# Optimization experiments

Hardware: AMD Instinct MI355X
Metric: run time of the kernel (lower is better)

The kernel has to match this reference:

```python
import jax, jax.numpy as jnp
import numpy as np

B, T, D, H, HS = 4, 1024, 1024, 16, 64
DW, DA, DG, DV = 64, 64, 128, 32
DM = H * HS  # == D here
EPS = 1e-5
DECAY_C = -0.606531  # -exp(-0.5)


def setup_inputs() -> dict:
    key = jax.random.key(0)
    ks = jax.random.split(key, 24)
    n = lambda k, s: jax.random.normal(k, s, dtype=jnp.float32)
    w = lambda k, s: n(k, s) * (1.0 / np.sqrt(s[0]))
    return dict(
        current=n(ks[0], (B, T, D)),
        prev=n(ks[1], (B, T, D)),
        v_first=n(ks[2], (B, T, DM)),
        rwkvag=jax.random.uniform(ks[3], (6, D), dtype=jnp.float32),
        rw_W=w(ks[4], (D, D)),
        w1=w(ks[5], (D, DW)), w2=w(ks[6], (DW, DM)), w2_b=n(ks[7], (DM,)) * 0.1,
        kw_W=w(ks[8], (D, DM)), vw_W=w(ks[9], (D, DM)),
        a1=w(ks[10], (D, DA)), a2=w(ks[11], (DA, DM)), a2_b=n(ks[12], (DM,)) * 0.1,
        v1=w(ks[13], (D, DV)), v2=w(ks[14], (DV, DM)), v2_b=n(ks[15], (DM,)) * 0.1,
        g1=w(ks[16], (D, DG)), g2=w(ks[17], (DG, DM)), g2_b=n(ks[18], (DM,)) * 0.1,
        k_k=jnp.ones((DM,)), k_a=jax.random.uniform(ks[19], (DM,), dtype=jnp.float32),
        r_k=jnp.ones((DM,)),
        gn_scale=jnp.ones((DM,)), gn_bias=jnp.zeros((DM,)),
        out_W=w(ks[20], (DM, D)),
    )


def _add_heads(x):
    return x.reshape(x.shape[:-1] + (H, HS))


def reference(current, prev, v_first, rwkvag, rw_W, w1, w2, w2_b, kw_W, vw_W,
              a1, a2, a2_b, v1, v2, v2_b, g1, g2, g2_b,
              k_k, k_a, r_k, gn_scale, gn_bias, out_W):
    diff = prev - current
    # per-channel token-shift mixing for the 6 branches: (B,T,6,D)
    x6 = current[..., None, :] + rwkvag * diff[..., None, :]
    xr, xw, xk, xv, xa, xg = (x6[..., i, :] for i in range(6))

    r = xr @ rw_W
    wl = jnp.tanh(xw @ w1) @ w2 + w2_b          # w-LoRA (tanh, bias_post)
    k = xk @ kw_W
    v = xv @ vw_W
    a = jax.nn.sigmoid((xa @ a1) @ a2 + a2_b)   # a-LoRA (bias_post) + sigmoid
    g = jax.nn.sigmoid(xg @ g1) @ g2 + g2_b     # g-LoRA (sigmoid act)

    kk = _add_heads(k * k_k)
    kk = kk / jnp.linalg.norm(kk, axis=-1, keepdims=True)
    k = k * (1.0 + (a - 1.0) * k_a)
    v = v + (v_first - v) * jax.nn.sigmoid((xv @ v1) @ v2 + v2_b)
    wdec = jnp.exp(DECAY_C * jax.nn.sigmoid(wl))  # decay in (exp(-0.6065), 1)

    rk_sum = _add_heads(r * k * r_k).sum(-1, keepdims=True)  # (B,T,H,1)
    rh, wh, kh, vh = _add_heads(r), _add_heads(wdec), _add_heads(k), _add_heads(v)
    at = -kk
    bt = kk * _add_heads(a)

    def step(state, xs):
        rt, wt, ktt, vt, att, btt = xs  # each (B,H,HS)
        sa = jnp.einsum('bhvk,bhk->bhv', state, att)
        state = (state * wt[:, :, None, :]
                 + sa[..., None] * btt[:, :, None, :]
                 + vt[..., None] * ktt[:, :, None, :])
        y = jnp.einsum('bhvk,bhk->bhv', state, rt)
        return state, y

    xs = tuple(jnp.moveaxis(x, 1, 0) for x in (rh, wh, kh, vh, at, bt))
    state0 = jnp.zeros((B, H, HS, HS), dtype=current.dtype)
    state, ys = jax.lax.scan(step, state0, xs)
    out = jnp.moveaxis(ys, 0, 1)  # (B,T,H,HS)

    # GroupNorm with n_head groups (normalize within each head)
    mu = out.mean(-1, keepdims=True)
    var = out.var(-1, keepdims=True)
    outn = (out - mu) * jax.lax.rsqrt(var + EPS)
    outn = outn.reshape(B, T, DM) * gn_scale + gn_bias

    outn = outn + (rk_sum * vh).reshape(B, T, DM)
    y = (outn * g) @ out_W
    return y, state, v_first
```

## Files before the change

### kernel.cpp

```cpp
#include <hip/hip_runtime.h>
#include <math.h>

#define NT 4096
#define DD 1024
#define NH 16
#define HSZ 64
#define GN_EPS 1e-5f
#define DECAY_C -0.606531f

typedef __attribute__((ext_vector_type(8))) short short8;
typedef __attribute__((ext_vector_type(4))) float float4v;

#define GLB(p) ((const __attribute__((address_space(1))) void*)(p))
#define LDS(p) ((__attribute__((address_space(3))) void*)(p))

__device__ __forceinline__ float sigm(float x) { return 1.f / (1.f + __expf(-x)); }

__device__ __forceinline__ unsigned short f2bf(float f) {
    unsigned int u = __float_as_uint(f);
    u = (u + 0x7fffu + ((u >> 16) & 1u)) >> 16;
    return (unsigned short)u;
}
__device__ __forceinline__ float bf2f(unsigned short h) {
    return __uint_as_float(((unsigned int)h) << 16);
}

__device__ __forceinline__ float row_sum16(float x) {
    int t;
    t = __builtin_amdgcn_update_dpp(0, __float_as_int(x), 0x128, 0xF, 0xF, true);
    x += __int_as_float(t);
    t = __builtin_amdgcn_update_dpp(0, __float_as_int(x), 0x124, 0xF, 0xF, true);
    x += __int_as_float(t);
    t = __builtin_amdgcn_update_dpp(0, __float_as_int(x), 0x122, 0xF, 0xF, true);
    x += __int_as_float(t);
    t = __builtin_amdgcn_update_dpp(0, __float_as_int(x), 0x121, 0xF, 0xF, true);
    x += __int_as_float(t);
    return x;
}

__global__ __launch_bounds__(256)
void mix6(const float* __restrict__ cur, const float* __restrict__ prev,
          const float* __restrict__ lam,
          ushort* __restrict__ xrh, ushort* __restrict__ xrl,
          ushort* __restrict__ xwh, ushort* __restrict__ xwl,
          ushort* __restrict__ xkh, ushort* __restrict__ xkl,
          ushort* __restrict__ xvh, ushort* __restrict__ xvl,
          ushort* __restrict__ xah, ushort* __restrict__ xal,
          ushort* __restrict__ xgh, ushort* __restrict__ xgl)
{
    const int tok = blockIdx.x;
    const int d0 = threadIdx.x * 4;
    const size_t base = (size_t)tok * DD + d0;
    float4 c = *(const float4*)(cur + base);
    float4 p = *(const float4*)(prev + base);
    float dx = p.x - c.x, dy = p.y - c.y, dz = p.z - c.z, dw = p.w - c.w;
    ushort* hs[6] = {xrh, xwh, xkh, xvh, xah, xgh};
    ushort* ls[6] = {xrl, xwl, xkl, xvl, xal, xgl};
#pragma unroll
    for (int j = 0; j < 6; j++) {
        float4 l = *(const float4*)(lam + j * DD + d0);
        float m0 = c.x + l.x * dx;
        float m1 = c.y + l.y * dy;
        float m2 = c.z + l.z * dz;
        float m3 = c.w + l.w * dw;
        ushort4 h;
        h.x = f2bf(m0); h.y = f2bf(m1); h.z = f2bf(m2); h.w = f2bf(m3);
        *(ushort4*)(hs[j] + base) = h;
        ushort4 lo;
        lo.x = f2bf(m0 - bf2f(h.x));
        lo.y = f2bf(m1 - bf2f(h.y));
        lo.z = f2bf(m2 - bf2f(h.z));
        lo.w = f2bf(m3 - bf2f(h.w));
        *(ushort4*)(ls[j] + base) = lo;
    }
}

__global__ __launch_bounds__(256)
void transpose_pad(const float* __restrict__ W, ushort* __restrict__ Wh,
                   ushort* __restrict__ Wl, int K, int N)
{
    __shared__ float tile[32][33];
    const int bx = blockIdx.x * 32;
    const int by = blockIdx.y * 32;
    const int tx = threadIdx.x, ty = threadIdx.y;
#pragma unroll
    for (int i = 0; i < 32; i += 8) {
        float v = 0.f;
        if (bx + tx < N) v = W[(size_t)(by + ty + i) * N + bx + tx];
        tile[ty + i][tx] = v;
    }
    __syncthreads();
#pragma unroll
    for (int i = 0; i < 32; i += 8) {
        float v = tile[tx][ty + i];
        ushort h = f2bf(v);
        size_t o = (size_t)(bx + ty + i) * K + by + tx;
        Wh[o] = h;
        if (Wl) Wl[o] = f2bf(v - bf2f(h));
    }
}

#define SWZ(r) (((r) >> 1) & 3)

__global__ __launch_bounds__(256)
void gemm_mega1(const ushort* __restrict__ xrh, const ushort* __restrict__ xrl,
                const ushort* __restrict__ xwh, const ushort* __restrict__ xwl,
                const ushort* __restrict__ xkh, const ushort* __restrict__ xkl,
                const ushort* __restrict__ xvh, const ushort* __restrict__ xvl,
                const ushort* __restrict__ xah, const ushort* __restrict__ xal,
                const ushort* __restrict__ xgh, const ushort* __restrict__ xgl,
                const ushort* __restrict__ Bth, const ushort* __restrict__ Btl,
                float* __restrict__ r_buf, float* __restrict__ k_buf,
                float* __restrict__ v_buf,
                ushort* __restrict__ hwh, ushort* __restrict__ hwl,
                ushort* __restrict__ hah, ushort* __restrict__ hal,
                ushort* __restrict__ hvh, ushort* __restrict__ hvl,
                ushort* __restrict__ hgh, ushort* __restrict__ hgl)
{
    __shared__ ushort AsH[128 * 32];
    __shared__ ushort BsH[128 * 32];
    __shared__ ushort AsL[128 * 32];
    __shared__ ushort BsL[128 * 32];
    const int cb = blockIdx.y;
    const ushort* Ah; const ushort* Al;
    if (cb < 8)       { Ah = xrh; Al = xrl; }
    else if (cb < 16) { Ah = xkh; Al = xkl; }
    else if (cb < 24) { Ah = xvh; Al = xvl; }
    else if (cb == 24){ Ah = xwh; Al = xwl; }
    else if (cb == 25){ Ah = xah; Al = xal; }
    else if (cb == 26){ Ah = xvh; Al = xvl; }
    else              { Ah = xgh; Al = xgl; }

    const int tid = threadIdx.x;
    const int rowBase = blockIdx.x * 128;
    const int colBase = cb * 128;
    const int lane = tid & 63;
    const int wave = tid >> 6;
    const int wm = wave >> 1, wn = wave & 1;
    const int m15 = lane & 15, quad = lane >> 4;

    float4v zero4 = {0.f, 0.f, 0.f, 0.f};
    float4v acc[4][4];
#pragma unroll
    for (int i = 0; i < 4; i++)
#pragma unroll
        for (int j = 0; j < 4; j++) acc[i][j] = zero4;

    for (int k0 = 0; k0 < 1024; k0 += 32) {
#pragma unroll
        for (int i = 0; i < 2; i++) {
            int idx = i * 256 + tid;
            int r = idx >> 2, seg = idx & 3;
            int sg = seg ^ SWZ(r);
            size_t aoff = (size_t)(rowBase + r) * 1024 + k0 + sg * 8;
            size_t boff = (size_t)(colBase + r) * 1024 + k0 + sg * 8;
            int dst = (i * 256 + (tid & ~63)) * 8;
            __builtin_amdgcn_global_load_lds(GLB(Ah + aoff), LDS(AsH + dst), 16, 0, 0);
            __builtin_amdgcn_global_load_lds(GLB(Bth + boff), LDS(BsH + dst), 16, 0, 0);
            __builtin_amdgcn_global_load_lds(GLB(Al + aoff), LDS(AsL + dst), 16, 0, 0);
            __builtin_amdgcn_global_load_lds(GLB(Btl + boff), LDS(BsL + dst), 16, 0, 0);
        }
        __syncthreads();
        short8 ah[4], bh[4], al[4], bl[4];
#pragma unroll
        for (int mi = 0; mi < 4; mi++) {
            int ra = wm * 64 + mi * 16 + m15;
            int cs = (quad ^ SWZ(ra)) * 8;
            ah[mi] = *(const short8*)(AsH + ra * 32 + cs);
            al[mi] = *(const short8*)(AsL + ra * 32 + cs);
        }
#pragma unroll
        for (int ni = 0; ni < 4; ni++) {
            int rb = wn * 64 + ni * 16 + m15;
            int cs = (quad ^ SWZ(rb)) * 8;
            bh[ni] = *(const short8*)(BsH + rb * 32 + cs);
            bl[ni] = *(const short8*)(BsL + rb * 32 + cs);
        }
#pragma unroll
        for (int mi = 0; mi < 4; mi++)
#pragma unroll
            for (int ni = 0; ni < 4; ni++) {
                acc[mi][ni] = __builtin_amdgcn_mfma_f32_16x16x32_bf16(al[mi], bh[ni], acc[mi][ni], 0, 0, 0);
                acc[mi][ni] = __builtin_amdgcn_mfma_f32_16x16x32_bf16(ah[mi], bl[ni], acc[mi][ni], 0, 0, 0);
                acc[mi][ni] = __builtin_amdgcn_mfma_f32_16x16x32_bf16(ah[mi], bh[ni], acc[mi][ni], 0, 0, 0);
            }
        __syncthreads();
    }

#pragma unroll
    for (int mi = 0; mi < 4; mi++) {
#pragma unroll
        for (int ni = 0; ni < 4; ni++) {
            int c = wn * 64 + ni * 16 + m15;
#pragma unroll
            for (int rr = 0; rr < 4; rr++) {
                int row = rowBase + wm * 64 + mi * 16 + quad * 4 + rr;
                float v = acc[mi][ni][rr];
                if (cb < 24) {
                    float* dst = (cb < 8) ? r_buf : (cb < 16) ? k_buf : v_buf;
                    int n = (cb & 7) * 128 + c;
                    dst[(size_t)row * 1024 + n] = v;
                } else if (cb == 24) {
                    if (c < 64) {
                        float t = tanhf(v);
                        ushort h = f2bf(t);
                        hwh[(size_t)row * 64 + c] = h;
                        hwl[(size_t)row * 64 + c] = f2bf(t - bf2f(h));
                    }
                } else if (cb == 25) {
                    if (c < 64) {
                        ushort h = f2bf(v);
                        hah[(size_t)row * 64 + c] = h;
                        hal[(size_t)row * 64 + c] = f2bf(v - bf2f(h));
                    }
                } else if (cb == 26) {
                    if (c < 32) {
                        ushort h = f2bf(v);
                        hvh[(size_t)row * 32 + c] = h;
                        hvl[(size_t)row * 32 + c] = f2bf(v - bf2f(h));
                    }
                } else {
                    float t = sigm(v);
                    ushort h = f2bf(t);
                    hgh[(size_t)row * 128 + c] = h;
                    hgl[(size_t)row * 128 + c] = f2bf(t - bf2f(h));
                }
            }
        }
    }
}

__global__ __launch_bounds__(256)
void gemm_mega2(const ushort* __restrict__ hwh, const ushort* __restrict__ hwl,
                const ushort* __restrict__ hah, const ushort* __restrict__ hal,
                const ushort* __restrict__ hvh, const ushort* __restrict__ hvl,
                const ushort* __restrict__ hgh, const ushort* __restrict__ hgl,
                const ushort* __restrict__ w2Th, const ushort* __restrict__ w2Tl,
                const ushort* __restrict__ a2Th, const ushort* __restrict__ a2Tl,
                const ushort* __restrict__ v2Th, const ushort* __restrict__ v2Tl,
                const ushort* __restrict__ g2Th, const ushort* __restrict__ g2Tl,
                const float* __restrict__ w2_b, const float* __restrict__ a2_b,
                const float* __restrict__ v2_b, const float* __restrict__ g2_b,
                float* __restrict__ w_buf, float* __restrict__ a_buf,
                float* __restrict__ vg_buf, float* __restrict__ g_buf)
{
    __shared__ ushort AsH[128 * 32];
    __shared__ ushort BsH[128 * 32];
    __shared__ ushort AsL[128 * 32];
    __shared__ ushort BsL[128 * 32];
    const int cb = blockIdx.y;
    const int seg = cb >> 3;
    const int K = (seg == 2) ? 32 : (seg == 3) ? 128 : 64;
    const ushort *Ah, *Al, *Bh, *Bl;
    const float* bias;
    float* outp;
    if (seg == 0) { Ah = hwh; Al = hwl; Bh = w2Th; Bl = w2Tl; bias = w2_b; outp = w_buf; }
    else if (seg == 1) { Ah = hah; Al = hal; Bh = a2Th; Bl = a2Tl; bias = a2_b; outp = a_buf; }
    else if (seg == 2) { Ah = hvh; Al = hvl; Bh = v2Th; Bl = v2Tl; bias = v2_b; outp = vg_buf; }
    else { Ah = hgh; Al = hgl; Bh = g2Th; Bl = g2Tl; bias = g2_b; outp = g_buf; }

    const int tid = threadIdx.x;
    const int rowBase = blockIdx.x * 128;
    const int colBase = (cb & 7) * 128;
    const int lane = tid & 63;
    const int wave = tid >> 6;
    const int wm = wave >> 1, wn = wave & 1;
    const int m15 = lane & 15, quad = lane >> 4;

    float4v zero4 = {0.f, 0.f, 0.f, 0.f};
    float4v acc[4][4];
#pragma unroll
    for (int i = 0; i < 4; i++)
#pragma unroll
        for (int j = 0; j < 4; j++) acc[i][j] = zero4;

    for (int k0 = 0; k0 < K; k0 += 32) {
#pragma unroll
        for (int i = 0; i < 2; i++) {
            int idx = i * 256 + tid;
            int r = idx >> 2, s8 = idx & 3;
            int sg = s8 ^ SWZ(r);
            size_t aoff = (size_t)(rowBase + r) * K + k0 + sg * 8;
            size_t boff = (size_t)(colBase + r) * K + k0 + sg * 8;
            int dst = (i * 256 + (tid & ~63)) * 8;
            __builtin_amdgcn_global_load_lds(GLB(Ah + aoff), LDS(AsH + dst), 16, 0, 0);
            __builtin_amdgcn_global_load_lds(GLB(Bh + boff), LDS(BsH + dst), 16, 0, 0);
            __builtin_amdgcn_global_load_lds(GLB(Al + aoff), LDS(AsL + dst), 16, 0, 0);
            __builtin_amdgcn_global_load_lds(GLB(Bl + boff), LDS(BsL + dst), 16, 0, 0);
        }
        __syncthreads();
        short8 ah[4], bh[4], al[4], bl[4];
#pragma unroll
        for (int mi = 0; mi < 4; mi++) {
            int ra = wm * 64 + mi * 16 + m15;
            int cs = (quad ^ SWZ(ra)) * 8;
            ah[mi] = *(const short8*)(AsH + ra * 32 + cs);
            al[mi] = *(const short8*)(AsL + ra * 32 + cs);
        }
#pragma unroll
        for (int ni = 0; ni < 4; ni++) {
            int rb = wn * 64 + ni * 16 + m15;
            int cs = (quad ^ SWZ(rb)) * 8;
            bh[ni] = *(const short8*)(BsH + rb * 32 + cs);
            bl[ni] = *(const short8*)(BsL + rb * 32 + cs);
        }
#pragma unroll
        for (int mi = 0; mi < 4; mi++)
#pragma unroll
            for (int ni = 0; ni < 4; ni++) {
                acc[mi][ni] = __builtin_amdgcn_mfma_f32_16x16x32_bf16(al[mi], bh[ni], acc[mi][ni], 0, 0, 0);
                acc[mi][ni] = __builtin_amdgcn_mfma_f32_16x16x32_bf16(ah[mi], bl[ni], acc[mi][ni], 0, 0, 0);
                acc[mi][ni] = __builtin_amdgcn_mfma_f32_16x16x32_bf16(ah[mi], bh[ni], acc[mi][ni], 0, 0, 0);
            }
        __syncthreads();
    }

#pragma unroll
    for (int mi = 0; mi < 4; mi++) {
#pragma unroll
        for (int ni = 0; ni < 4; ni++) {
            int col = colBase + wn * 64 + ni * 16 + m15;
            float bv = bias[col];
#pragma unroll
            for (int rr = 0; rr < 4; rr++) {
                int row = rowBase + wm * 64 + mi * 16 + quad * 4 + rr;
                float v = acc[mi][ni][rr] + bv;
                if (seg == 1 || seg == 2) v = sigm(v);
                outp[(size_t)row * 1024 + col] = v;
            }
        }
    }
}

__global__ __launch_bounds__(256)
void gemm_bf16s(const ushort* __restrict__ Ah, const ushort* __restrict__ Bh,
                float* __restrict__ outF, int N, int K)
{
    __shared__ ushort AsH[128 * 32];
    __shared__ ushort BsH[128 * 32];
    const int tid = threadIdx.x;
    const int rowBase = blockIdx.x * 128;
    const int colBase = blockIdx.y * 128;
    const int lane = tid & 63;
    const int wave = tid >> 6;
    const int wm = wave >> 1, wn = wave & 1;
    const int m15 = lane & 15, quad = lane >> 4;

    float4v zero4 = {0.f, 0.f, 0.f, 0.f};
    float4v acc[4][4];
#pragma unroll
    for (int i = 0; i < 4; i++)
#pragma unroll
        for (int j = 0; j < 4; j++) acc[i][j] = zero4;

    for (int k0 = 0; k0 < K; k0 += 32) {
#pragma unroll
        for (int i = 0; i < 2; i++) {
            int idx = i * 256 + tid;
            int r = idx >> 2, seg = idx & 3;
            int sg = seg ^ SWZ(r);
            size_t aoff = (size_t)(rowBase + r) * K + k0 + sg * 8;
            size_t boff = (size_t)(colBase + r) * K + k0 + sg * 8;
            int dst = (i * 256 + (tid & ~63)) * 8;
            __builtin_amdgcn_global_load_lds(GLB(Ah + aoff), LDS(AsH + dst), 16, 0, 0);
            __builtin_amdgcn_global_load_lds(GLB(Bh + boff), LDS(BsH + dst), 16, 0, 0);
        }
        __syncthreads();
        short8 ah[4], bh[4];
#pragma unroll
        for (int mi = 0; mi < 4; mi++) {
            int ra = wm * 64 + mi * 16 + m15;
            ah[mi] = *(const short8*)(AsH + ra * 32 + (quad ^ SWZ(ra)) * 8);
        }
#pragma unroll
        for (int ni = 0; ni < 4; ni++) {
            int rb = wn * 64 + ni * 16 + m15;
            bh[ni] = *(const short8*)(BsH + rb * 32 + (quad ^ SWZ(rb)) * 8);
        }
#pragma unroll
        for (int mi = 0; mi < 4; mi++)
#pragma unroll
            for (int ni = 0; ni < 4; ni++)
                acc[mi][ni] = __builtin_amdgcn_mfma_f32_16x16x32_bf16(ah[mi], bh[ni], acc[mi][ni], 0, 0, 0);
        __syncthreads();
    }

#pragma unroll
    for (int mi = 0; mi < 4; mi++) {
#pragma unroll
        for (int ni = 0; ni < 4; ni++) {
            int col = colBase + wn * 64 + ni * 16 + m15;
#pragma unroll
            for (int rr = 0; rr < 4; rr++) {
                int row = rowBase + wm * 64 + mi * 16 + quad * 4 + rr;
                outF[(size_t)row * N + col] = acc[mi][ni][rr];
            }
        }
    }
}

__global__ __launch_bounds__(256)
void elemwise1(const float* __restrict__ r_buf, float* __restrict__ wl_buf,
               float* __restrict__ k_buf, float* __restrict__ v_buf,
               float* __restrict__ kkn_buf, const float* __restrict__ a_buf,
               const float* __restrict__ vg_buf, const float* __restrict__ vfirst,
               const float* __restrict__ kkw, const float* __restrict__ kaw,
               const float* __restrict__ rkw, float* __restrict__ rk_sum)
{
    const int tok = blockIdx.x;
    const int tid = threadIdx.x;
    const int d0 = tid * 4;
    const size_t base = (size_t)tok * DD + d0;

    float4 k0 = *(const float4*)(k_buf + base);
    float4 a4 = *(const float4*)(a_buf + base);
    float4 wl = *(const float4*)(wl_buf + base);
    float4 v0 = *(const float4*)(v_buf + base);
    float4 vg = *(const float4*)(vg_buf + base);
    float4 vf = *(const float4*)(vfirst + base);
    float4 r4 = *(const float4*)(r_buf + base);
    float4 kkc = *(const float4*)(kkw + d0);
    float4 kac = *(const float4*)(kaw + d0);
    float4 rkc = *(const float4*)(rkw + d0);

    float kk0 = k0.x * kkc.x, kk1 = k0.y * kkc.y, kk2 = k0.z * kkc.z, kk3 = k0.w * kkc.w;
    float ss = kk0 * kk0 + kk1 * kk1 + kk2 * kk2 + kk3 * kk3;
    ss += __shfl_xor(ss, 1); ss += __shfl_xor(ss, 2);
    ss += __shfl_xor(ss, 4); ss += __shfl_xor(ss, 8);
    float rn = rsqrtf(ss);
    float4 kkn = { kk0 * rn, kk1 * rn, kk2 * rn, kk3 * rn };
    *(float4*)(kkn_buf + base) = kkn;

    float4 kf;
    kf.x = k0.x * (1.f + (a4.x - 1.f) * kac.x);
    kf.y = k0.y * (1.f + (a4.y - 1.f) * kac.y);
    kf.z = k0.z * (1.f + (a4.z - 1.f) * kac.z);
    kf.w = k0.w * (1.f + (a4.w - 1.f) * kac.w);
    *(float4*)(k_buf + base) = kf;

    float rk = r4.x * kf.x * rkc.x + r4.y * kf.y * rkc.y + r4.z * kf.z * rkc.z + r4.w * kf.w * rkc.w;
    rk += __shfl_xor(rk, 1); rk += __shfl_xor(rk, 2);
    rk += __shfl_xor(rk, 4); rk += __shfl_xor(rk, 8);
    if ((tid & 15) == 0) rk_sum[(size_t)tok * NH + (tid >> 4)] = rk;

    float4 vfin;
    vfin.x = v0.x + (vf.x - v0.x) * vg.x;
    vfin.y = v0.y + (vf.y - v0.y) * vg.y;
    vfin.z = v0.z + (vf.z - v0.z) * vg.z;
    vfin.w = v0.w + (vf.w - v0.w) * vg.w;
    *(float4*)(v_buf + base) = vfin;

    float4 wd;
    wd.x = __expf(DECAY_C * sigm(wl.x));
    wd.y = __expf(DECAY_C * sigm(wl.y));
    wd.z = __expf(DECAY_C * sigm(wl.z));
    wd.w = __expf(DECAY_C * sigm(wl.w));
    *(float4*)(wl_buf + base) = wd;
}

__global__ __launch_bounds__(256)
void scan_kernel(const float* __restrict__ r_buf, const float* __restrict__ w_buf,
                 const float* __restrict__ k_buf, const float* __restrict__ kkn_buf,
                 const float* __restrict__ a_buf, const float* __restrict__ v_buf,
                 float* __restrict__ out_scan, float* __restrict__ state_out)
{
    __shared__ float vecJ[2][5][16][64];
    __shared__ float vbuf2[2][16][16];
    __shared__ float ypart[2][16][16][16];
    const int bh = blockIdx.x;
    const int rg = blockIdx.y;
    const int b = bh >> 4, h = bh & 15;
    const int tid = threadIdx.x;
    const int row = tid >> 4, l16 = tid & 15;
    const int lofs = l16 * 4;
    const int rowbase = rg * 16;
    const size_t tok0 = ((size_t)b * 1024) * DD + h * HSZ;
    float s0 = 0.f, s1 = 0.f, s2 = 0.f, s3 = 0.f;

#define STAGE(cc, bb) do {                                                        \
    const int tt_ = tid >> 4;                                                     \
    const int dd4_ = (tid & 15) * 4;                                              \
    size_t gofs_ = tok0 + (size_t)((cc) * 16 + tt_) * DD + dd4_;                  \
    float* db_ = &vecJ[bb][0][0][0] + ((tid >> 6) << 8);                          \
    __builtin_amdgcn_global_load_lds(GLB(r_buf + gofs_),   LDS(db_),        16, 0, 0); \
    __builtin_amdgcn_global_load_lds(GLB(w_buf + gofs_),   LDS(db_ + 1024), 16, 0, 0); \
    __builtin_amdgcn_global_load_lds(GLB(k_buf + gofs_),   LDS(db_ + 2048), 16, 0, 0); \
    __builtin_amdgcn_global_load_lds(GLB(kkn_buf + gofs_), LDS(db_ + 3072), 16, 0, 0); \
    __builtin_amdgcn_global_load_lds(GLB(a_buf + gofs_),   LDS(db_ + 4096), 16, 0, 0); \
    if (tid < 64) {                                                               \
        size_t vofs_ = tok0 + (size_t)((cc) * 16 + (tid >> 2)) * DD + rowbase + (tid & 3) * 4; \
        __builtin_amdgcn_global_load_lds(GLB(v_buf + vofs_), LDS(&vbuf2[bb][0][0]), 16, 0, 0); \
    }                                                                             \
} while (0)

#define LD_TOK(P, tt) do {                                                        \
    P##r = *(const float4*)(vb + (tt) * 64 + lofs);                               \
    P##w = *(const float4*)(vb + 1024 + (tt) * 64 + lofs);                        \
    P##k = *(const float4*)(vb + 2048 + (tt) * 64 + lofs);                        \
    P##q = *(const float4*)(vb + 3072 + (tt) * 64 + lofs);                        \
    P##a = *(const float4*)(vb + 4096 + (tt) * 64 + lofs);                        \
    P##v = vbp[(tt) * 16 + row];                                                  \
} while (0)

#define STEP(P, tt) do {                                                          \
    float sa_ = P##q.x * s0;                                                      \
    sa_ = fmaf(P##q.y, s1, sa_);                                                  \
    sa_ = fmaf(P##q.z, s2, sa_);                                                  \
    sa_ = fmaf(P##q.w, s3, sa_);                                                  \
    sa_ = row_sum16(sa_);                                                         \
    float n0_ = P##q.x * P##a.x, n1_ = P##q.y * P##a.y;                           \
    float n2_ = P##q.z * P##a.z, n3_ = P##q.w * P##a.w;                           \
    float b0_ = fmaf(s0, P##w.x, P##v * P##k.x);                                  \
    float b1_ = fmaf(s1, P##w.y, P##v * P##k.y);                                  \
    float b2_ = fmaf(s2, P##w.z, P##v * P##k.z);                                  \
    float b3_ = fmaf(s3, P##w.w, P##v * P##k.w);                                  \
    s0 = fmaf(sa_, -n0_, b0_);                                                    \
    s1 = fmaf(sa_, -n1_, b1_);                                                    \
    s2 = fmaf(sa_, -n2_, b2_);                                                    \
    s3 = fmaf(sa_, -n3_, b3_);                                                    \
    float yp_ = P##r.x * s0;                                                      \
    yp_ = fmaf(P##r.y, s1, yp_);                                                  \
    yp_ = fmaf(P##r.z, s2, yp_);                                                  \
    yp_ = fmaf(P##r.w, s3, yp_);                                                  \
    ypart[buf][tt][row][l16] = yp_;                                               \
} while (0)

    STAGE(0, 0);
    __syncthreads();

    for (int c = 0; c < 64; c++) {
        const int buf = c & 1;
        if (c < 63) STAGE(c + 1, buf ^ 1);
        const float* vb  = &vecJ[buf][0][0][0];
        const float* vbp = &vbuf2[buf][0][0];
        float4 Ar, Aw, Ak, Aq, Aa; float Av;
        float4 Br, Bw, Bk, Bq, Ba; float Bv;
        LD_TOK(A, 0);
#pragma unroll
        for (int tp = 0; tp < 8; tp++) {
            LD_TOK(B, 2 * tp + 1);
            STEP(A, 2 * tp);
            if (tp < 7) LD_TOK(A, 2 * tp + 2);
            STEP(B, 2 * tp + 1);
        }
        __syncthreads();
        {
            const int t_ = tid >> 4, r_ = tid & 15;
            const float* yp = &ypart[buf][t_][r_][0];
            float4 y0 = *(const float4*)(yp);
            float4 y1 = *(const float4*)(yp + 4);
            float4 y2 = *(const float4*)(yp + 8);
            float4 y3 = *(const float4*)(yp + 12);
            float ys = ((y0.x + y0.y) + (y0.z + y0.w)) + ((y1.x + y1.y) + (y1.z + y1.w))
                     + ((y2.x + y2.y) + (y2.z + y2.w)) + ((y3.x + y3.y) + (y3.z + y3.w));
            out_scan[tok0 + (size_t)(c * 16 + t_) * DD + rowbase + r_] = ys;
        }
    }

#undef STAGE
#undef LD_TOK
#undef STEP

    float* so = state_out + ((size_t)(b * NH + h) * HSZ + rowbase + row) * HSZ + l16 * 4;
    float4 sv = {s0, s1, s2, s3};
    *(float4*)so = sv;
}

__global__ __launch_bounds__(256)
void elemwise2(const float* __restrict__ out_scan, const float* __restrict__ rk_sum,
               const float* __restrict__ v_buf, const float* __restrict__ g_buf,
               const float* __restrict__ gscale, const float* __restrict__ gbias,
               ushort* __restrict__ z_buf)
{
    const int tok = blockIdx.x;
    const int tid = threadIdx.x;
    const int d0 = tid * 4;
    const size_t base = (size_t)tok * DD + d0;

    float4 o = *(const float4*)(out_scan + base);
    float sm = o.x + o.y + o.z + o.w;
    float ss = o.x * o.x + o.y * o.y + o.z * o.z + o.w * o.w;
    sm += __shfl_xor(sm, 1); sm += __shfl_xor(sm, 2);
    sm += __shfl_xor(sm, 4); sm += __shfl_xor(sm, 8);
    ss += __shfl_xor(ss, 1); ss += __shfl_xor(ss, 2);
    ss += __shfl_xor(ss, 4); ss += __shfl_xor(ss, 8);
    float mu = sm * (1.f / 64.f);
    float var = ss * (1.f / 64.f) - mu * mu;
    float rs = rsqrtf(var + GN_EPS);
    float rk = rk_sum[(size_t)tok * NH + (tid >> 4)];

    float4 v4 = *(const float4*)(v_buf + base);
    float4 g4 = *(const float4*)(g_buf + base);
    float4 gs = *(const float4*)(gscale + d0);
    float4 gb = *(const float4*)(gbias + d0);
    ushort4 z;
    z.x = f2bf(((o.x - mu) * rs * gs.x + gb.x + rk * v4.x) * g4.x);
    z.y = f2bf(((o.y - mu) * rs * gs.y + gb.y + rk * v4.y) * g4.y);
    z.z = f2bf(((o.z - mu) * rs * gs.z + gb.z + rk * v4.z) * g4.z);
    z.w = f2bf(((o.w - mu) * rs * gs.w + gb.w + rk * v4.w) * g4.w);
    *(ushort4*)(z_buf + base) = z;
}

extern "C" void kernel_launch(void* const* d_in, const int* in_sizes, int n_in,
                              void* d_out, int out_size, void* d_ws, size_t ws_size,
                              hipStream_t stream) {
    const float* cur    = (const float*)d_in[0];
    const float* prev   = (const float*)d_in[1];
    const float* vfirst = (const float*)d_in[2];
    const float* rwkvag = (const float*)d_in[3];
    const float* rw_W   = (const float*)d_in[4];
    const float* w1     = (const float*)d_in[5];
    const float* w2     = (const float*)d_in[6];
    const float* w2_b   = (const float*)d_in[7];
    const float* kw_W   = (const float*)d_in[8];
    const float* vw_W   = (const float*)d_in[9];
    const float* a1     = (const float*)d_in[10];
    const float* a2     = (const float*)d_in[11];
    const float* a2_b   = (const float*)d_in[12];
    const float* v1     = (const float*)d_in[13];
    const float* v2     = (const float*)d_in[14];
    const float* v2_b   = (const float*)d_in[15];
    const float* g1     = (const float*)d_in[16];
    const float* g2     = (const float*)d_in[17];
    const float* g2_b   = (const float*)d_in[18];
    const float* k_k    = (const float*)d_in[19];
    const float* k_a    = (const float*)d_in[20];
    const float* r_k    = (const float*)d_in[21];
    const float* gn_s   = (const float*)d_in[22];
    const float* gn_b   = (const float*)d_in[23];
    const float* out_W  = (const float*)d_in[24];

    float* out = (float*)d_out;
    float* y_out = out;
    float* state_out = out + (size_t)NT * DD;
    float* vf_out = state_out + (size_t)4 * NH * HSZ * HSZ;

    float* p = (float*)d_ws;
    const size_t big = (size_t)NT * DD;
    const size_t half = big / 2;
    float* r_buf = p;   p += big;
    float* k_buf = p;   p += big;
    float* v_buf = p;   p += big;
    float* xreg = p;
    ushort* xrh = (ushort*)(xreg);            ushort* xrl = (ushort*)(xreg + half);
    ushort* xwh = (ushort*)(xreg + 2*half);   ushort* xwl = (ushort*)(xreg + 3*half);
    ushort* xkh = (ushort*)(xreg + 4*half);   ushort* xkl = (ushort*)(xreg + 5*half);
    ushort* xvh = (ushort*)(xreg + 6*half);   ushort* xvl = (ushort*)(xreg + 7*half);
    ushort* xah = (ushort*)(xreg + 8*half);   ushort* xal = (ushort*)(xreg + 9*half);
    ushort* xgh = (ushort*)(xreg + 10*half);  ushort* xgl = (ushort*)(xreg + 11*half);
    p += 12 * half;
    float* w_buf   = xreg + 0 * half;
    float* a_buf   = xreg + 2 * half;
    float* vg_buf  = xreg + 4 * half;
    float* os_buf  = vg_buf;
    float* g_buf   = xreg + 6 * half;
    float* kkn_buf = xreg + 8 * half;
    float* btreg = p;
    ushort* Bth = (ushort*)btreg;
    ushort* Btl = (ushort*)(btreg + 1835008);
    p += 2 * 1835008;
    ushort* z_bf  = (ushort*)btreg;
    ushort* outTh = (ushort*)(btreg + 2097152);
    ushort* w2Th = (ushort*)p; p += 32768; ushort* w2Tl = (ushort*)p; p += 32768;
    ushort* a2Th = (ushort*)p; p += 32768; ushort* a2Tl = (ushort*)p; p += 32768;
    ushort* v2Th = (ushort*)p; p += 16384; ushort* v2Tl = (ushort*)p; p += 16384;
    ushort* g2Th = (ushort*)p; p += 65536; ushort* g2Tl = (ushort*)p; p += 65536;
    ushort* hwh = (ushort*)p; p += 131072; ushort* hwl = (ushort*)p; p += 131072;
    ushort* hah = (ushort*)p; p += 131072; ushort* hal = (ushort*)p; p += 131072;
    ushort* hvh = (ushort*)p; p += 65536;  ushort* hvl = (ushort*)p; p += 65536;
    ushort* hgh = (ushort*)p; p += 262144; ushort* hgl = (ushort*)p; p += 262144;
    float* rks_buf = p;        p += 65536;

    dim3 blk(256);
    dim3 t32x8(32, 8);

    transpose_pad<<<dim3(32, 32), t32x8, 0, stream>>>(rw_W, Bth + (size_t)0 * 1024,    Btl + (size_t)0 * 1024,    1024, 1024);
    transpose_pad<<<dim3(32, 32), t32x8, 0, stream>>>(kw_W, Bth + (size_t)1024 * 1024, Btl + (size_t)1024 * 1024, 1024, 1024);
    transpose_pad<<<dim3(32, 32), t32x8, 0, stream>>>(vw_W, Bth + (size_t)2048 * 1024, Btl + (size_t)2048 * 1024, 1024, 1024);
    transpose_pad<<<dim3(4, 32), t32x8, 0, stream>>>(w1, Bth + (size_t)3072 * 1024, Btl + (size_t)3072 * 1024, 1024, 64);
    transpose_pad<<<dim3(4, 32), t32x8, 0, stream>>>(a1, Bth + (size_t)3200 * 1024, Btl + (size_t)3200 * 1024, 1024, 64);
    transpose_pad<<<dim3(4, 32), t32x8, 0, stream>>>(v1, Bth + (size_t)3328 * 1024, Btl + (size_t)3328 * 1024, 1024, 32);
    transpose_pad<<<dim3(4, 32), t32x8, 0, stream>>>(g1, Bth + (size_t)3456 * 1024, Btl + (size_t)3456 * 1024, 1024, 128);
    transpose_pad<<<dim3(32, 2), t32x8, 0, stream>>>(w2, w2Th, w2Tl, 64, 1024);
    transpose_pad<<<dim3(32, 2), t32x8, 0, stream>>>(a2, a2Th, a2Tl, 64, 1024);
    transpose_pad<<<dim3(32, 1), t32x8, 0, stream>>>(v2, v2Th, v2Tl, 32, 1024);
    transpose_pad<<<dim3(32, 4), t32x8, 0, stream>>>(g2, g2Th, g2Tl, 128, 1024);

    mix6<<<NT, blk, 0, stream>>>(cur, prev, rwkvag,
                                 xrh, xrl, xwh, xwl, xkh, xkl,
                                 xvh, xvl, xah, xal, xgh, xgl);

    gemm_mega1<<<dim3(32, 28), blk, 0, stream>>>(
        xrh, xrl, xwh, xwl, xkh, xkl, xvh, xvl, xah, xal, xgh, xgl,
        Bth, Btl, r_buf, k_buf, v_buf,
        hwh, hwl, hah, hal, hvh, hvl, hgh, hgl);

    transpose_pad<<<dim3(32, 32), t32x8, 0, stream>>>(out_W, outTh, nullptr, 1024, 1024);

    gemm_mega2<<<dim3(32, 32), blk, 0, stream>>>(
        hwh, hwl, hah, hal, hvh, hvl, hgh, hgl,
        w2Th, w2Tl, a2Th, a2Tl, v2Th, v2Tl, g2Th, g2Tl,
        w2_b, a2_b, v2_b, g2_b,
        w_buf, a_buf, vg_buf, g_buf);

    elemwise1<<<NT, blk, 0, stream>>>(r_buf, w_buf, k_buf, v_buf, kkn_buf, a_buf,
                                      vg_buf, vfirst, k_k, k_a, r_k, rks_buf);

    scan_kernel<<<dim3(64, 4), blk, 0, stream>>>(r_buf, w_buf, k_buf, kkn_buf, a_buf, v_buf,
                                                 os_buf, state_out);

    elemwise2<<<NT, blk, 0, stream>>>(os_buf, rks_buf, v_buf, g_buf, gn_s, gn_b, z_bf);

    gemm_bf16s<<<dim3(32, 8), blk, 0, stream>>>(z_bf, outTh, y_out, 1024, 1024);

    hipMemcpyAsync(vf_out, vfirst, (size_t)NT * DD * sizeof(float),
                   hipMemcpyDeviceToDevice, stream);
}
```

Measured before the change: 536.7 us.

## Enlarge gemm_mega1 tiles to 256x256 with double-buffered LDS prefetch

The fused first-stage GEMM moves from 128x128 tiles with 256 threads to 256x256 tiles with 512 threads. Each wave now computes a 128x64 sub-tile, and the LDS staging is double-buffered so the next K-slice loads while MFMAs run on the current one. The goal is more operand reuse per byte loaded, fewer blocks, and global-load latency hidden behind compute. In exchange, the small LoRA projections are padded to 256 columns, which adds wasted MFMA work. Each thread holds 128 accumulator floats under a 512-thread, 2-block launch bound, so register spilling or low occupancy is a risk, and LDS use rises to 128 KB per block.

```diff
diff --git a/kernel.cpp b/kernel.cpp
--- a/kernel.cpp
+++ b/kernel.cpp
@@ -102,7 +102,7 @@
 
 #define SWZ(r) (((r) >> 1) & 3)
 
-__global__ __launch_bounds__(256)
+__global__ __launch_bounds__(512, 2)
 void gemm_mega1(const ushort* __restrict__ xrh, const ushort* __restrict__ xrl,
                 const ushort* __restrict__ xwh, const ushort* __restrict__ xwl,
                 const ushort* __restrict__ xkh, const ushort* __restrict__ xkl,
@@ -117,113 +117,127 @@
                 ushort* __restrict__ hvh, ushort* __restrict__ hvl,
                 ushort* __restrict__ hgh, ushort* __restrict__ hgl)
 {
-    __shared__ ushort AsH[128 * 32];
-    __shared__ ushort BsH[128 * 32];
-    __shared__ ushort AsL[128 * 32];
-    __shared__ ushort BsL[128 * 32];
-    const int cb = blockIdx.y;
+    __shared__ ushort As[2][2][256 * 32];
+    __shared__ ushort Bs[2][2][256 * 32];
+    const int ct = blockIdx.y;
     const ushort* Ah; const ushort* Al;
-    if (cb < 8)       { Ah = xrh; Al = xrl; }
-    else if (cb < 16) { Ah = xkh; Al = xkl; }
-    else if (cb < 24) { Ah = xvh; Al = xvl; }
-    else if (cb == 24){ Ah = xwh; Al = xwl; }
-    else if (cb == 25){ Ah = xah; Al = xal; }
-    else if (cb == 26){ Ah = xvh; Al = xvl; }
+    if (ct < 4)       { Ah = xrh; Al = xrl; }
+    else if (ct < 8)  { Ah = xkh; Al = xkl; }
+    else if (ct < 12) { Ah = xvh; Al = xvl; }
+    else if (ct == 12){ Ah = xwh; Al = xwl; }
+    else if (ct == 13){ Ah = xah; Al = xal; }
+    else if (ct == 14){ Ah = xvh; Al = xvl; }
     else              { Ah = xgh; Al = xgl; }
 
     const int tid = threadIdx.x;
-    const int rowBase = blockIdx.x * 128;
-    const int colBase = cb * 128;
+    const int rowBase = blockIdx.x * 256;
+    const int colBase = ct * 256;
     const int lane = tid & 63;
     const int wave = tid >> 6;
-    const int wm = wave >> 1, wn = wave & 1;
+    const int wm = wave >> 2, wn = wave & 3;
     const int m15 = lane & 15, quad = lane >> 4;
 
     float4v zero4 = {0.f, 0.f, 0.f, 0.f};
-    float4v acc[4][4];
-#pragma unroll
-    for (int i = 0; i < 4; i++)
+    float4v acc[8][4];
+#pragma unroll
+    for (int i = 0; i < 8; i++)
 #pragma unroll
         for (int j = 0; j < 4; j++) acc[i][j] = zero4;
 
-    for (int k0 = 0; k0 < 1024; k0 += 32) {
-#pragma unroll
-        for (int i = 0; i < 2; i++) {
-            int idx = i * 256 + tid;
-            int r = idx >> 2, seg = idx & 3;
-            int sg = seg ^ SWZ(r);
-            size_t aoff = (size_t)(rowBase + r) * 1024 + k0 + sg * 8;
-            size_t boff = (size_t)(colBase + r) * 1024 + k0 + sg * 8;
-            int dst = (i * 256 + (tid & ~63)) * 8;
-            __builtin_amdgcn_global_load_lds(GLB(Ah + aoff), LDS(AsH + dst), 16, 0, 0);
-            __builtin_amdgcn_global_load_lds(GLB(Bth + boff), LDS(BsH + dst), 16, 0, 0);
-            __builtin_amdgcn_global_load_lds(GLB(Al + aoff), LDS(AsL + dst), 16, 0, 0);
-            __builtin_amdgcn_global_load_lds(GLB(Btl + boff), LDS(BsL + dst), 16, 0, 0);
-        }
-        __syncthreads();
-        short8 ah[4], bh[4], al[4], bl[4];
-#pragma unroll
-        for (int mi = 0; mi < 4; mi++) {
-            int ra = wm * 64 + mi * 16 + m15;
-            int cs = (quad ^ SWZ(ra)) * 8;
-            ah[mi] = *(const short8*)(AsH + ra * 32 + cs);
-            al[mi] = *(const short8*)(AsL + ra * 32 + cs);
-        }
+#define STAGE1(kk, bb) do {                                                       \
+    const int k0_ = (kk) * 32;                                                    \
+    _Pragma("unroll")                                                             \
+    for (int i_ = 0; i_ < 2; i_++) {                                              \
+        int idx_ = i_ * 512 + tid;                                                \
+        int r_ = idx_ >> 2, seg_ = idx_ & 3;                                      \
+        int sg_ = seg_ ^ SWZ(r_);       \
+        size_t aoff_ = (size_t)(rowBase + r_) * 1024 + k0_ + sg_ * 8;             \
+        size_t boff_ = (size_t)(colBase + r_) * 1024 + k0_ + sg_ * 8;             \
+        int dst_ = (i_ * 512 + (tid & ~63)) * 8;                                  \
+        __builtin_amdgcn_global_load_lds(GLB(Ah + aoff_),  LDS(&As[bb][0][0] + dst_), 16, 0, 0); \
+        __builtin_amdgcn_global_load_lds(GLB(Al + aoff_),  LDS(&As[bb][1][0] + dst_), 16, 0, 0); \
+        __builtin_amdgcn_global_load_lds(GLB(Bth + boff_), LDS(&Bs[bb][0][0] + dst_), 16, 0, 0); \
+        __builtin_amdgcn_global_load_lds(GLB(Btl + boff_), LDS(&Bs[bb][1][0] + dst_), 16, 0, 0); \
+    }                                                                             \
+} while (0)
+
+    STAGE1(0, 0);
+    __syncthreads();
+
+    for (int kt = 0; kt < 32; kt++) {
+        const int buf = kt & 1;
+        if (kt < 31) STAGE1(kt + 1, buf ^ 1);
+
+        short8 bh[4], bl[4];
 #pragma unroll
         for (int ni = 0; ni < 4; ni++) {
             int rb = wn * 64 + ni * 16 + m15;
             int cs = (quad ^ SWZ(rb)) * 8;
-            bh[ni] = *(const short8*)(BsH + rb * 32 + cs);
-            bl[ni] = *(const short8*)(BsL + rb * 32 + cs);
-        }
-#pragma unroll
-        for (int mi = 0; mi < 4; mi++)
-#pragma unroll
-            for (int ni = 0; ni < 4; ni++) {
-                acc[mi][ni] = __builtin_amdgcn_mfma_f32_16x16x32_bf16(al[mi], bh[ni], acc[mi][ni], 0, 0, 0);
-                acc[mi][ni] = __builtin_amdgcn_mfma_f32_16x16x32_bf16(ah[mi], bl[ni], acc[mi][ni], 0, 0, 0);
-                acc[mi][ni] = __builtin_amdgcn_mfma_f32_16x16x32_bf16(ah[mi], bh[ni], acc[mi][ni], 0, 0, 0);
+            bh[ni] = *(const short8*)(&Bs[buf][0][0] + rb * 32 + cs);
+            bl[ni] = *(const short8*)(&Bs[buf][1][0] + rb * 32 + cs);
+        }
+#pragma unroll
+        for (int h2 = 0; h2 < 2; h2++) {
+            short8 ah[4], al[4];
+#pragma unroll
+            for (int mi = 0; mi < 4; mi++) {
+                int ra = wm * 128 + (h2 * 4 + mi) * 16 + m15;
+                int cs = (quad ^ SWZ(ra)) * 8;
+                ah[mi] = *(const short8*)(&As[buf][0][0] + ra * 32 + cs);
+                al[mi] = *(const short8*)(&As[buf][1][0] + ra * 32 + cs);
             }
+#pragma unroll
+            for (int mi = 0; mi < 4; mi++)
+#pragma unroll
+                for (int ni = 0; ni < 4; ni++) {
+                    acc[h2*4+mi][ni] = __builtin_amdgcn_mfma_f32_16x16x32_bf16(al[mi], bh[ni], acc[h2*4+mi][ni], 0, 0, 0);
+                    acc[h2*4+mi][ni] = __builtin_amdgcn_mfma_f32_16x16x32_bf16(ah[mi], bl[ni], acc[h2*4+mi][ni], 0, 0, 0);
+                    acc[h2*4+mi][ni] = __builtin_amdgcn_mfma_f32_16x16x32_bf16(ah[mi], bh[ni], acc[h2*4+mi][ni], 0, 0, 0);
+                }
+        }
         __syncthreads();
     }
-
-#pragma unroll
-    for (int mi = 0; mi < 4; mi++) {
+#undef STAGE1
+
+#pragma unroll
+    for (int mi = 0; mi < 8; mi++) {
 #pragma unroll
         for (int ni = 0; ni < 4; ni++) {
             int c = wn * 64 + ni * 16 + m15;
 #pragma unroll
             for (int rr = 0; rr < 4; rr++) {
-                int row = rowBase + wm * 64 + mi * 16 + quad * 4 + rr;
+                int row = rowBase + wm * 128 + mi * 16 + quad * 4 + rr;
                 float v = acc[mi][ni][rr];
-                if (cb < 24) {
-                    float* dst = (cb < 8) ? r_buf : (cb < 16) ? k_buf : v_buf;
-                    int n = (cb & 7) * 128 + c;
+                if (ct < 12) {
+                    float* dst = (ct < 4) ? r_buf : (ct < 8) ? k_buf : v_buf;
+                    int n = (ct & 3) * 256 + c;
                     dst[(size_t)row * 1024 + n] = v;
-                } else if (cb == 24) {
+                } else if (ct == 12) {
                     if (c < 64) {
                         float t = tanhf(v);
                         ushort h = f2bf(t);
                         hwh[(size_t)row * 64 + c] = h;
                         hwl[(size_t)row * 64 + c] = f2bf(t - bf2f(h));
                     }
-                } else if (cb == 25) {
+                } else if (ct == 13) {
                     if (c < 64) {
                         ushort h = f2bf(v);
                         hah[(size_t)row * 64 + c] = h;
                         hal[(size_t)row * 64 + c] = f2bf(v - bf2f(h));
                     }
-                } else if (cb == 26) {
+                } else if (ct == 14) {
                     if (c < 32) {
                         ushort h = f2bf(v);
                         hvh[(size_t)row * 32 + c] = h;
                         hvl[(size_t)row * 32 + c] = f2bf(v - bf2f(h));
                     }
                 } else {
-                    float t = sigm(v);
-                    ushort h = f2bf(t);
-                    hgh[(size_t)row * 128 + c] = h;
-                    hgl[(size_t)row * 128 + c] = f2bf(t - bf2f(h));
+                    if (c < 128) {
+                        float t = sigm(v);
+                        ushort h = f2bf(t);
+                        hgh[(size_t)row * 128 + c] = h;
+                        hgl[(size_t)row * 128 + c] = f2bf(t - bf2f(h));
+                    }
                 }
             }
         }
@@ -657,8 +671,8 @@
     float* kkn_buf = xreg + 8 * half;
     float* btreg = p;
     ushort* Bth = (ushort*)btreg;
-    ushort* Btl = (ushort*)(btreg + 1835008);
-    p += 2 * 1835008;
+    ushort* Btl = (ushort*)(btreg + 2097152);
+    p += 2 * 2097152;
     ushort* z_bf  = (ushort*)btreg;
     ushort* outTh = (ushort*)(btreg + 2097152);
     ushort* w2Th = (ushort*)p; p += 32768; ushort* w2Tl = (ushort*)p; p += 32768;
@@ -677,10 +691,10 @@
     transpose_pad<<<dim3(32, 32), t32x8, 0, stream>>>(rw_W, Bth + (size_t)0 * 1024,    Btl + (size_t)0 * 1024,    1024, 1024);
     transpose_pad<<<dim3(32, 32), t32x8, 0, stream>>>(kw_W, Bth + (size_t)1024 * 1024, Btl + (size_t)1024 * 1024, 1024, 1024);
     transpose_pad<<<dim3(32, 32), t32x8, 0, stream>>>(vw_W, Bth + (size_t)2048 * 1024, Btl + (size_t)2048 * 1024, 1024, 1024);
-    transpose_pad<<<dim3(4, 32), t32x8, 0, stream>>>(w1, Bth + (size_t)3072 * 1024, Btl + (size_t)3072 * 1024, 1024, 64);
-    transpose_pad<<<dim3(4, 32), t32x8, 0, stream>>>(a1, Bth + (size_t)3200 * 1024, Btl + (size_t)3200 * 1024, 1024, 64);
-    transpose_pad<<<dim3(4, 32), t32x8, 0, stream>>>(v1, Bth + (size_t)3328 * 1024, Btl + (size_t)3328 * 1024, 1024, 32);
-    transpose_pad<<<dim3(4, 32), t32x8, 0, stream>>>(g1, Bth + (size_t)3456 * 1024, Btl + (size_t)3456 * 1024, 1024, 128);
+    transpose_pad<<<dim3(8, 32), t32x8, 0, stream>>>(w1, Bth + (size_t)3072 * 1024, Btl + (size_t)3072 * 1024, 1024, 64);
+    transpose_pad<<<dim3(8, 32), t32x8, 0, stream>>>(a1, Bth + (size_t)3328 * 1024, Btl + (size_t)3328 * 1024, 1024, 64);
+    transpose_pad<<<dim3(8, 32), t32x8, 0, stream>>>(v1, Bth + (size_t)3584 * 1024, Btl + (size_t)3584 * 1024, 1024, 32);
+    transpose_pad<<<dim3(8, 32), t32x8, 0, stream>>>(g1, Bth + (size_t)3840 * 1024, Btl + (size_t)3840 * 1024, 1024, 128);
     transpose_pad<<<dim3(32, 2), t32x8, 0, stream>>>(w2, w2Th, w2Tl, 64, 1024);
     transpose_pad<<<dim3(32, 2), t32x8, 0, stream>>>(a2, a2Th, a2Tl, 64, 1024);
     transpose_pad<<<dim3(32, 1), t32x8, 0, stream>>>(v2, v2Th, v2Tl, 32, 1024);
@@ -690,7 +704,7 @@
                                  xrh, xrl, xwh, xwl, xkh, xkl,
                                  xvh, xvl, xah, xal, xgh, xgl);
 
-    gemm_mega1<<<dim3(32, 28), blk, 0, stream>>>(
+    gemm_mega1<<<dim3(16, 16), dim3(512), 0, stream>>>(
         xrh, xrl, xwh, xwl, xkh, xkl, xvh, xvl, xah, xal, xgh, xgl,
         Bth, Btl, r_buf, k_buf, v_buf,
         hwh, hwl, hah, hal, hvh, hvl, hgh, hgl);
```

New measurement: 850.8 us. +58.5%, slower.

## Double-buffer LDS tiles in the projection and output GEMMs

Applied to the files above, without the earlier changes.

Both MFMA GEMM kernels get two LDS buffers. The global-to-LDS loads for the next K tile are issued before the MFMAs on the current tile, so memory latency overlaps compute and only one barrier is needed per iteration. The cost is double the shared memory per block (64 KB in the split-bf16 mega kernel), which can lower how many blocks fit on each CU.

```diff
diff --git a/kernel.cpp b/kernel.cpp
--- a/kernel.cpp
+++ b/kernel.cpp
@@ -117,10 +117,8 @@
                 ushort* __restrict__ hvh, ushort* __restrict__ hvl,
                 ushort* __restrict__ hgh, ushort* __restrict__ hgl)
 {
-    __shared__ ushort AsH[128 * 32];
-    __shared__ ushort BsH[128 * 32];
-    __shared__ ushort AsL[128 * 32];
-    __shared__ ushort BsL[128 * 32];
+    __shared__ ushort As[2][2][128 * 32];
+    __shared__ ushort Bs[2][2][128 * 32];
     const int cb = blockIdx.y;
     const ushort* Ah; const ushort* Al;
     if (cb < 8)       { Ah = xrh; Al = xrl; }
@@ -146,35 +144,44 @@
 #pragma unroll
         for (int j = 0; j < 4; j++) acc[i][j] = zero4;
 
-    for (int k0 = 0; k0 < 1024; k0 += 32) {
-#pragma unroll
-        for (int i = 0; i < 2; i++) {
-            int idx = i * 256 + tid;
-            int r = idx >> 2, seg = idx & 3;
-            int sg = seg ^ SWZ(r);
-            size_t aoff = (size_t)(rowBase + r) * 1024 + k0 + sg * 8;
-            size_t boff = (size_t)(colBase + r) * 1024 + k0 + sg * 8;
-            int dst = (i * 256 + (tid & ~63)) * 8;
-            __builtin_amdgcn_global_load_lds(GLB(Ah + aoff), LDS(AsH + dst), 16, 0, 0);
-            __builtin_amdgcn_global_load_lds(GLB(Bth + boff), LDS(BsH + dst), 16, 0, 0);
-            __builtin_amdgcn_global_load_lds(GLB(Al + aoff), LDS(AsL + dst), 16, 0, 0);
-            __builtin_amdgcn_global_load_lds(GLB(Btl + boff), LDS(BsL + dst), 16, 0, 0);
-        }
-        __syncthreads();
+#define STAGE1(kk, bb) do {                                                       \
+    const int k0_ = (kk) * 32;                                                    \
+    _Pragma("unroll")                                                             \
+    for (int i_ = 0; i_ < 2; i_++) {                                              \
+        int idx_ = i_ * 256 + tid;                                                \
+        int r_ = idx_ >> 2, seg_ = idx_ & 3;                                      \
+        int sg_ = seg_ ^ SWZ(r_);       \
+        size_t aoff_ = (size_t)(rowBase + r_) * 1024 + k0_ + sg_ * 8;             \
+        size_t boff_ = (size_t)(colBase + r_) * 1024 + k0_ + sg_ * 8;             \
+        int dst_ = (i_ * 256 + (tid & ~63)) * 8;                                  \
+        __builtin_amdgcn_global_load_lds(GLB(Ah + aoff_),  LDS(&As[bb][0][0] + dst_), 16, 0, 0); \
+        __builtin_amdgcn_global_load_lds(GLB(Al + aoff_),  LDS(&As[bb][1][0] + dst_), 16, 0, 0); \
+        __builtin_amdgcn_global_load_lds(GLB(Bth + boff_), LDS(&Bs[bb][0][0] + dst_), 16, 0, 0); \
+        __builtin_amdgcn_global_load_lds(GLB(Btl + boff_), LDS(&Bs[bb][1][0] + dst_), 16, 0, 0); \
+    }                                                                             \
+} while (0)
+
+    STAGE1(0, 0);
+    __syncthreads();
+
+    for (int kt = 0; kt < 32; kt++) {
+        const int buf = kt & 1;
+        if (kt < 31) STAGE1(kt + 1, buf ^ 1);
+
         short8 ah[4], bh[4], al[4], bl[4];
 #pragma unroll
         for (int mi = 0; mi < 4; mi++) {
             int ra = wm * 64 + mi * 16 + m15;
             int cs = (quad ^ SWZ(ra)) * 8;
-            ah[mi] = *(const short8*)(AsH + ra * 32 + cs);
-            al[mi] = *(const short8*)(AsL + ra * 32 + cs);
+            ah[mi] = *(const short8*)(&As[buf][0][0] + ra * 32 + cs);
+            al[mi] = *(const short8*)(&As[buf][1][0] + ra * 32 + cs);
         }
 #pragma unroll
         for (int ni = 0; ni < 4; ni++) {
             int rb = wn * 64 + ni * 16 + m15;
             int cs = (quad ^ SWZ(rb)) * 8;
-            bh[ni] = *(const short8*)(BsH + rb * 32 + cs);
-            bl[ni] = *(const short8*)(BsL + rb * 32 + cs);
+            bh[ni] = *(const short8*)(&Bs[buf][0][0] + rb * 32 + cs);
+            bl[ni] = *(const short8*)(&Bs[buf][1][0] + rb * 32 + cs);
         }
 #pragma unroll
         for (int mi = 0; mi < 4; mi++)
@@ -186,6 +193,7 @@
             }
         __syncthreads();
     }
+#undef STAGE1
 
 #pragma unroll
     for (int mi = 0; mi < 4; mi++) {
@@ -336,8 +344,8 @@
 void gemm_bf16s(const ushort* __restrict__ Ah, const ushort* __restrict__ Bh,
                 float* __restrict__ outF, int N, int K)
 {
-    __shared__ ushort AsH[128 * 32];
-    __shared__ ushort BsH[128 * 32];
+    __shared__ ushort As2[2][128 * 32];
+    __shared__ ushort Bs2[2][128 * 32];
     const int tid = threadIdx.x;
     const int rowBase = blockIdx.x * 128;
     const int colBase = blockIdx.y * 128;
@@ -353,29 +361,38 @@
 #pragma unroll
         for (int j = 0; j < 4; j++) acc[i][j] = zero4;
 
-    for (int k0 = 0; k0 < K; k0 += 32) {
-#pragma unroll
-        for (int i = 0; i < 2; i++) {
-            int idx = i * 256 + tid;
-            int r = idx >> 2, seg = idx & 3;
-            int sg = seg ^ SWZ(r);
-            size_t aoff = (size_t)(rowBase + r) * K + k0 + sg * 8;
-            size_t boff = (size_t)(colBase + r) * K + k0 + sg * 8;
-            int dst = (i * 256 + (tid & ~63)) * 8;
-            __builtin_amdgcn_global_load_lds(GLB(Ah + aoff), LDS(AsH + dst), 16, 0, 0);
-            __builtin_amdgcn_global_load_lds(GLB(Bh + boff), LDS(BsH + dst), 16, 0, 0);
-        }
-        __syncthreads();
+#define STAGE3(kk, bb) do {                                                       \
+    const int k0_ = (kk) * 32;                                                    \
+    _Pragma("unroll")                                                             \
+    for (int i_ = 0; i_ < 2; i_++) {                                              \
+        int idx_ = i_ * 256 + tid;                                                \
+        int r_ = idx_ >> 2, seg_ = idx_ & 3;                                      \
+        int sg_ = seg_ ^ SWZ(r_);                                                 \
+        size_t aoff_ = (size_t)(rowBase + r_) * K + k0_ + sg_ * 8;                \
+        size_t boff_ = (size_t)(colBase + r_) * K + k0_ + sg_ * 8;                \
+        int dst_ = (i_ * 256 + (tid & ~63)) * 8;                                  \
+        __builtin_amdgcn_global_load_lds(GLB(Ah + aoff_), LDS(&As2[bb][0] + dst_), 16, 0, 0); \
+        __builtin_amdgcn_global_load_lds(GLB(Bh + boff_), LDS(&Bs2[bb][0] + dst_), 16, 0, 0); \
+    }                                                                             \
+} while (0)
+
+    const int nk = K >> 5;
+    STAGE3(0, 0);
+    __syncthreads();
+
+    for (int kt = 0; kt < nk; kt++) {
+        const int buf = kt & 1;
+        if (kt < nk - 1) STAGE3(kt + 1, buf ^ 1);
         short8 ah[4], bh[4];
 #pragma unroll
         for (int mi = 0; mi < 4; mi++) {
             int ra = wm * 64 + mi * 16 + m15;
-            ah[mi] = *(const short8*)(AsH + ra * 32 + (quad ^ SWZ(ra)) * 8);
+            ah[mi] = *(const short8*)(&As2[buf][0] + ra * 32 + (quad ^ SWZ(ra)) * 8);
         }
 #pragma unroll
         for (int ni = 0; ni < 4; ni++) {
             int rb = wn * 64 + ni * 16 + m15;
-            bh[ni] = *(const short8*)(BsH + rb * 32 + (quad ^ SWZ(rb)) * 8);
+            bh[ni] = *(const short8*)(&Bs2[buf][0] + rb * 32 + (quad ^ SWZ(rb)) * 8);
         }
 #pragma unroll
         for (int mi = 0; mi < 4; mi++)
@@ -384,6 +401,7 @@
                 acc[mi][ni] = __builtin_amdgcn_mfma_f32_16x16x32_bf16(ah[mi], bh[ni], acc[mi][ni], 0, 0, 0);
         __syncthreads();
     }
+#undef STAGE3
 
 #pragma unroll
     for (int mi = 0; mi < 4; mi++) {
```

Measured after the change: 543.0 us. About the same (+1.2%).
